# Kernel optimization log

Measured on AMD Instinct MI355X. Metric: run time of the kernel, lower is better.

## Reference

```python
import jax, jax.numpy as jnp
import numpy as np

B, S, H, DH = 2, 2048, 16, 64
DIM = H * DH          # 1024
WIN = 512             # relpos_win_size
LN_EPS = 1e-5


def setup_inputs() -> dict:
    key = jax.random.key(0)
    ks = jax.random.split(key, 8)
    return {
        "q": jax.random.normal(ks[0], (B, S, H, DH), dtype=jnp.float32),
        "k": jax.random.normal(ks[1], (B, S, H, DH), dtype=jnp.float32),
        "relpos_emb": jax.random.normal(ks[2], (WIN, DIM), dtype=jnp.float32),
        "ln_scale": jnp.ones((DIM,), dtype=jnp.float32),
        "ln_bias": jnp.zeros((DIM,), dtype=jnp.float32),
        "Wq": jax.random.normal(ks[3], (DIM, DIM), dtype=jnp.float32),
        "bq": jnp.zeros((DIM,), dtype=jnp.float32),
        "Wk": jax.random.normal(ks[4], (DIM, DIM), dtype=jnp.float32),
        "bk": jnp.zeros((DIM,), dtype=jnp.float32),
    }


def reference(q, k, relpos_emb, ln_scale, ln_bias, Wq, bq, Wk, bk):
    b, nq, h, dh = q.shape
    nk = k.shape[1]
    win = relpos_emb.shape[0]

    # LayerNorm over the embedding dim (use_pos_layer_norm=True); dropout is identity (eval).
    mu = jnp.mean(relpos_emb, axis=-1, keepdims=True)
    var = jnp.mean(jnp.square(relpos_emb - mu), axis=-1, keepdims=True)
    pe = (relpos_emb - mu) * jax.lax.rsqrt(var + LN_EPS) * ln_scale + ln_bias

    qpos = jnp.arange(nq)
    kpos = jnp.arange(nk)
    rel = jnp.clip(kpos[None, :] - qpos[:, None], -(win - 1), 0) + (win - 1)
    idx = jnp.broadcast_to(rel[None, None, :, :], (b, h, nq, nk))

    # Linear projections of the (small) relpos table, split into heads.
    relpos_k = (pe @ Wk.T + bk).reshape(win, h, dh)  # relpos_k_proj
    relpos_q = (pe @ Wq.T + bq).reshape(win, h, dh)  # relpos_q_proj

    # query-to-position: scores over window then gather along window axis (dim 3).
    query_pos_scores = jnp.einsum('bnhx,khx->bhnk', q, relpos_k)
    logits_query_pos = jnp.take_along_axis(query_pos_scores, idx, axis=3)  # [b,h,nq,nk]

    key_pos_scores = jnp.einsum('bnhx,khx->bhkn', k, relpos_q)
    logits_pos_key = jnp.take_along_axis(key_pos_scores, idx, axis=2)      # [b,h,nq,nk]

    # scale_factor = 1 + True + True = 3 (static constant, omitted from array outputs)
    return logits_pos_key, logits_query_pos, relpos_q, relpos_k
```

## Files before the change

kernel.cpp:

```cpp
#include <hip/hip_runtime.h>

#define BB 2
#define S 2048
#define H 16
#define DH 64
#define DIM 1024
#define WIN 512

#define OUT_PK 0
#define OUT_QP 134217728
#define OUT_RQ 268435456
#define OUT_RK 268959744

#define WS_C0Q   1024
#define WS_C511Q (1024 + 65536)
#define WS_C0K   (1024 + 2*65536)
#define WS_C511K (1024 + 3*65536)
#define WS_BF_BASE 263168

typedef short bf16x8 __attribute__((ext_vector_type(8)));
typedef float f32x4 __attribute__((ext_vector_type(4)));

__device__ inline short f2bf(float f) {
    union { float f; unsigned int u; } cv; cv.f = f;
    unsigned int u = cv.u + 0x7FFFu + ((cv.u >> 16) & 1u);
    return (short)(u >> 16);
}

__device__ inline float bf2f(short s) {
    union { unsigned int u; float f; } cv;
    cv.u = ((unsigned int)(unsigned short)s) << 16;
    return cv.f;
}

__global__ __launch_bounds__(256) void proj(const float* __restrict__ emb,
        const float* __restrict__ lnsc, const float* __restrict__ lnbi,
        const float* __restrict__ Wq, const float* __restrict__ bq,
        const float* __restrict__ Wk, const float* __restrict__ bk,
        float* __restrict__ out, short* __restrict__ rqbf, short* __restrict__ rkbf) {
    const float* W    = blockIdx.z ? Wk : Wq;
    const float* bias = blockIdx.z ? bk : bq;
    float* o = out + (blockIdx.z ? OUT_RK : OUT_RQ);
    short* bfo = blockIdx.z ? rkbf : rqbf;
    int r0 = blockIdx.x * 64;
    int d0 = blockIdx.y * 64;
    __shared__ short As[64 * 72];
    __shared__ short Bs[64 * 72];
    __shared__ float smu[64];
    __shared__ float srs[64];
    int t = threadIdx.x;

    {
        int rr = t >> 2, p = t & 3;
        const float4* rp = reinterpret_cast<const float4*>(emb + (r0 + rr) * DIM + p * 256);
        float s = 0.f, sq = 0.f;
#pragma unroll
        for (int i = 0; i < 64; ++i) {
            float4 v = rp[i];
            s  += v.x + v.y + v.z + v.w;
            sq += v.x * v.x + v.y * v.y + v.z * v.z + v.w * v.w;
        }
        s += __shfl_xor(s, 1); sq += __shfl_xor(sq, 1);
        s += __shfl_xor(s, 2); sq += __shfl_xor(sq, 2);
        if (p == 0) {
            float mu = s / DIM;
            float var = sq / DIM - mu * mu;
            smu[rr] = mu;
            srs[rr] = rsqrtf(var + 1e-5f);
        }
    }
    __syncthreads();

    int lane = t & 63, w = t >> 6, lr = lane & 15, lg = lane >> 4;
    int srow = t >> 2, seg = (t & 3) * 16;
    float mu = smu[srow], rs = srs[srow];

    f32x4 acc[4] = {};
    for (int c0 = 0; c0 < DIM; c0 += 64) {
        const float4* ep = reinterpret_cast<const float4*>(emb + (size_t)(r0 + srow) * DIM + c0 + seg);
        const float4* wp = reinterpret_cast<const float4*>(W + (size_t)(d0 + srow) * DIM + c0 + seg);
        short4* ad = reinterpret_cast<short4*>(&As[srow * 72 + seg]);
        short4* wd = reinterpret_cast<short4*>(&Bs[srow * 72 + seg]);
#pragma unroll
        for (int i = 0; i < 4; ++i) {
            float4 v = ep[i], wv = wp[i];
            int cb = c0 + seg + i * 4;
            float4 sc = *reinterpret_cast<const float4*>(lnsc + cb);
            float4 bi = *reinterpret_cast<const float4*>(lnbi + cb);
            short4 a4 = { f2bf((v.x - mu) * rs * sc.x + bi.x),
                          f2bf((v.y - mu) * rs * sc.y + bi.y),
                          f2bf((v.z - mu) * rs * sc.z + bi.z),
                          f2bf((v.w - mu) * rs * sc.w + bi.w) };
            short4 w4 = { f2bf(wv.x), f2bf(wv.y), f2bf(wv.z), f2bf(wv.w) };
            ad[i] = a4;
            wd[i] = w4;
        }
        __syncthreads();
#pragma unroll
        for (int kk = 0; kk < 2; ++kk) {
            bf16x8 a = *reinterpret_cast<const bf16x8*>(&As[(w * 16 + lr) * 72 + kk * 32 + lg * 8]);
#pragma unroll
            for (int cg = 0; cg < 4; ++cg) {
                bf16x8 b = *reinterpret_cast<const bf16x8*>(&Bs[(cg * 16 + lr) * 72 + kk * 32 + lg * 8]);
                acc[cg] = __builtin_amdgcn_mfma_f32_16x16x32_bf16(a, b, acc[cg], 0, 0, 0);
            }
        }
        __syncthreads();
    }
#pragma unroll
    for (int cg = 0; cg < 4; ++cg) {
        int col = d0 + cg * 16 + lr;
        float bv = bias[col];
        int hh = col >> 6, cc = col & 63;
#pragma unroll
        for (int reg = 0; reg < 4; ++reg) {
            int rr = r0 + w * 16 + lg * 4 + reg;
            float val = acc[cg][reg] + bv;
            o[(size_t)rr * DIM + col] = val;
            bfo[((size_t)(hh * 512) + rr) * 64 + cc] = f2bf(val);
        }
    }
}

__global__ __launch_bounds__(256) void qkprep(const float* __restrict__ q,
        const float* __restrict__ k, const float* __restrict__ out_ro,
        float* __restrict__ ws, short* __restrict__ qbf, short* __restrict__ kbf) {
    int z = blockIdx.z;
    int bh = blockIdx.y; int b = bh >> 4, h = bh & 15;
    int row = blockIdx.x * 64 + (threadIdx.x >> 2);
    int seg = (threadIdx.x & 3) * 16;
    const float* X = z ? k : q;
    const float* T = out_ro + (z ? OUT_RQ : OUT_RK);
    short* dst = z ? kbf : qbf;
    const float4* xp = reinterpret_cast<const float4*>(X + (size_t)((b * S + row) * H + h) * DH + seg);
    const float4* t0 = reinterpret_cast<const float4*>(T + h * DH + seg);
    const float4* t1 = reinterpret_cast<const float4*>(T + 511 * DIM + h * DH + seg);
    float d0 = 0.f, d1 = 0.f;
    short* dbase = dst + ((size_t)bh * 2048 + row) * 64 + seg;
#pragma unroll
    for (int i = 0; i < 4; ++i) {
        float4 x = xp[i], a = t0[i], c = t1[i];
        d0 += x.x * a.x + x.y * a.y + x.z * a.z + x.w * a.w;
        d1 += x.x * c.x + x.y * c.y + x.z * c.z + x.w * c.w;
        short4 o = { f2bf(x.x), f2bf(x.y), f2bf(x.z), f2bf(x.w) };
        *reinterpret_cast<short4*>(dbase + i * 4) = o;
    }
    d0 += __shfl_xor(d0, 1); d0 += __shfl_xor(d0, 2);
    d1 += __shfl_xor(d1, 1); d1 += __shfl_xor(d1, 2);
    if ((threadIdx.x & 3) == 0) {
        int o = bh * S + row;
        if (!z) { ws[WS_C0Q + o] = d0; ws[WS_C511Q + o] = d1; }
        else    { ws[WS_C0K + o] = d0; ws[WS_C511K + o] = d1; }
    }
}

__global__ __launch_bounds__(256) void outk(const short* __restrict__ qbf,
        const short* __restrict__ kbf, const short* __restrict__ rqbf,
        const short* __restrict__ rkbf, const float* __restrict__ ws,
        float* __restrict__ out) {
    __shared__ short Yt[64 * 132];

    int bid = blockIdx.x;
    int wg = (bid & 7) * 8192 + (bid >> 3);
    int PK = wg >> 15;
    int bh = (wg >> 10) & 31; int h = bh & 15;
    int nt = (wg >> 5) & 31, jt = wg & 31;
    int n0 = nt * 64, j0 = jt * 64;
    int jlo = nt > 8 ? nt - 8 : 0;
    int t = threadIdx.x;
    float* obase = out + (PK ? OUT_PK : OUT_QP) + (size_t)bh * S * S;

    if (jt < jlo || jt > nt) {
        int left = jt < jlo;
        const float* cv = ws + (PK ? (left ? WS_C0K : WS_C511K)
                                   : (left ? WS_C0Q : WS_C511Q)) + bh * S;
        int col4 = t & 15, r0w = t >> 4;
        if (PK) {
            f32x4 v = *reinterpret_cast<const f32x4*>(cv + j0 + col4 * 4);
#pragma unroll
            for (int i = 0; i < 4; ++i) {
                int n = n0 + r0w + i * 16;
                __builtin_nontemporal_store(v,
                    reinterpret_cast<f32x4*>(obase + (size_t)n * S + j0 + col4 * 4));
            }
        } else {
#pragma unroll
            for (int i = 0; i < 4; ++i) {
                int n = n0 + r0w + i * 16;
                float vs = cv[n];
                f32x4 v = { vs, vs, vs, vs };
                __builtin_nontemporal_store(v,
                    reinterpret_cast<f32x4*>(obase + (size_t)n * S + j0 + col4 * 4));
            }
        }
        return;
    }

    int rlo = 511 + j0 - (n0 + 63); rlo = rlo < 0 ? 0 : rlo;

    const short* xb = (PK ? kbf : qbf) + ((size_t)bh * 2048 + (PK ? j0 : n0)) * 64;
    const short* tbase = (PK ? rqbf : rkbf) + (size_t)h * 512 * 64;

    int lane = t & 63, w = t >> 6, lr = lane & 15, lg = lane >> 4;
    const short* arow = xb + (w * 16 + lr) * 64 + lg * 8;
    bf16x8 a0 = *reinterpret_cast<const bf16x8*>(arow);
    bf16x8 a1 = *reinterpret_cast<const bf16x8*>(arow + 32);

    bf16x8 b0s[8], b1s[8];
#pragma unroll
    for (int s = 0; s < 8; ++s) {
        int trow = rlo + s * 16 + lr;
        trow = trow > 511 ? 511 : trow;
        const short* brow = tbase + trow * 64 + lg * 8;
        b0s[s] = *reinterpret_cast<const bf16x8*>(brow);
        b1s[s] = *reinterpret_cast<const bf16x8*>(brow + 32);
    }
#pragma unroll
    for (int s = 0; s < 8; ++s) {
        f32x4 acc = {0.f, 0.f, 0.f, 0.f};
        acc = __builtin_amdgcn_mfma_f32_16x16x32_bf16(a0, b0s[s], acc, 0, 0, 0);
        acc = __builtin_amdgcn_mfma_f32_16x16x32_bf16(a1, b1s[s], acc, 0, 0, 0);
#pragma unroll
        for (int reg = 0; reg < 4; ++reg)
            Yt[(w * 16 + lg * 4 + reg) * 132 + s * 16 + lr] = f2bf(acc[reg]);
    }
    __syncthreads();

    int tx = t & 15, ty = t >> 4;
#pragma unroll
    for (int i = 0; i < 4; ++i) {
        int rowi = ty + i * 16;
        int n = n0 + rowi;
        float vv[4];
#pragma unroll
        for (int jj = 0; jj < 4; ++jj) {
            int j = j0 + tx * 4 + jj;
            int rel = 511 + j - n;
            rel = rel < 0 ? 0 : (rel > 511 ? 511 : rel);
            int g = rel - rlo;
            int m = PK ? (tx * 4 + jj) : rowi;
            vv[jj] = bf2f(Yt[m * 132 + g]);
        }
        f32x4 v = { vv[0], vv[1], vv[2], vv[3] };
        __builtin_nontemporal_store(v,
            reinterpret_cast<f32x4*>(obase + (size_t)n * S + j0 + tx * 4));
    }
}

extern "C" void kernel_launch(void* const* d_in, const int* in_sizes, int n_in,
                              void* d_out, int out_size, void* d_ws, size_t ws_size,
                              hipStream_t stream) {
    const float* q    = (const float*)d_in[0];
    const float* k    = (const float*)d_in[1];
    const float* emb  = (const float*)d_in[2];
    const float* lnsc = (const float*)d_in[3];
    const float* lnbi = (const float*)d_in[4];
    const float* Wq   = (const float*)d_in[5];
    const float* bq   = (const float*)d_in[6];
    const float* Wk   = (const float*)d_in[7];
    const float* bk   = (const float*)d_in[8];
    float* out = (float*)d_out;
    float* ws  = (float*)d_ws;

    short* qbf  = (short*)(ws + WS_BF_BASE);
    short* kbf  = qbf + (size_t)4194304;
    short* rqbf = kbf + (size_t)4194304;
    short* rkbf = rqbf + (size_t)524288;

    proj<<<dim3(8, 16, 2), dim3(256), 0, stream>>>(emb, lnsc, lnbi, Wq, bq, Wk, bk, out, rqbf, rkbf);
    qkprep<<<dim3(32, 32, 2), dim3(256), 0, stream>>>(q, k, out, ws, qbf, kbf);
    outk<<<dim3(65536), dim3(256), 0, stream>>>(qbf, kbf, rqbf, rkbf, ws, out);
}
```

Measured before the change: 234.6 us.

## Restructure work split: merge q/k bf16 conversion into projection, flat-fill row blocks

The q/k bf16 conversion now runs in the same launch as the relpos projection, and the edge-value dot products move to a separate small kernel that reads the bf16 copies. The output kernel now launches only band tiles (enumerated triangularly) plus flat work items that each fill the constant regions of 8 full rows, instead of one block per 64x64 tile. The LDS scratch tile is transposed so each lane writes a packed short4. This is meant to cut launch count and per-block overhead on the large constant-fill region. In exchange the edge values are now computed from bf16 inputs rather than fp32, which loses some precision.

Measured after the change: 310.6 us. +32.4%, slower.

```diff
diff --git a/kernel.cpp b/kernel.cpp
--- a/kernel.cpp
+++ b/kernel.cpp
@@ -33,22 +33,44 @@
     return cv.f;
 }
 
-__global__ __launch_bounds__(256) void proj(const float* __restrict__ emb,
+__global__ __launch_bounds__(256) void prep1(const float* __restrict__ emb,
         const float* __restrict__ lnsc, const float* __restrict__ lnbi,
         const float* __restrict__ Wq, const float* __restrict__ bq,
         const float* __restrict__ Wk, const float* __restrict__ bk,
-        float* __restrict__ out, short* __restrict__ rqbf, short* __restrict__ rkbf) {
-    const float* W    = blockIdx.z ? Wk : Wq;
-    const float* bias = blockIdx.z ? bk : bq;
-    float* o = out + (blockIdx.z ? OUT_RK : OUT_RQ);
-    short* bfo = blockIdx.z ? rkbf : rqbf;
-    int r0 = blockIdx.x * 64;
-    int d0 = blockIdx.y * 64;
+        const float* __restrict__ q, const float* __restrict__ k,
+        float* __restrict__ out, short* __restrict__ rqbf, short* __restrict__ rkbf,
+        short* __restrict__ qbf, short* __restrict__ kbf) {
     __shared__ short As[64 * 72];
     __shared__ short Bs[64 * 72];
     __shared__ float smu[64];
     __shared__ float srs[64];
+    int bid = blockIdx.x;
     int t = threadIdx.x;
+
+    if (bid >= 256) {
+        int cb = bid - 256;
+        int z = cb >> 10;
+        int blk = cb & 1023;
+        const float* src = z ? k : q;
+        short* dst = z ? kbf : qbf;
+        int e0 = (blk * 256 + t) * 16;
+        int c = e0 & 63, hh = (e0 >> 6) & 15, n = (e0 >> 10) & 2047, b = e0 >> 21;
+        short* dbase = dst + (((size_t)(b * 16 + hh) * 2048) + n) * 64 + c;
+#pragma unroll
+        for (int i = 0; i < 4; ++i) {
+            float4 v = *reinterpret_cast<const float4*>(src + e0 + i * 4);
+            short4 o = { f2bf(v.x), f2bf(v.y), f2bf(v.z), f2bf(v.w) };
+            *reinterpret_cast<short4*>(dbase + i * 4) = o;
+        }
+        return;
+    }
+
+    const float* W    = (bid >> 7) ? Wk : Wq;
+    const float* bias = (bid >> 7) ? bk : bq;
+    float* o = out + ((bid >> 7) ? OUT_RK : OUT_RQ);
+    short* bfo = (bid >> 7) ? rkbf : rqbf;
+    int r0 = (bid & 7) * 64;
+    int d0 = ((bid >> 3) & 15) * 64;
 
     {
         int rr = t >> 2, p = t & 3;
@@ -84,9 +106,9 @@
 #pragma unroll
         for (int i = 0; i < 4; ++i) {
             float4 v = ep[i], wv = wp[i];
-            int cb = c0 + seg + i * 4;
-            float4 sc = *reinterpret_cast<const float4*>(lnsc + cb);
-            float4 bi = *reinterpret_cast<const float4*>(lnbi + cb);
+            int cb2 = c0 + seg + i * 4;
+            float4 sc = *reinterpret_cast<const float4*>(lnsc + cb2);
+            float4 bi = *reinterpret_cast<const float4*>(lnbi + cb2);
             short4 a4 = { f2bf((v.x - mu) * rs * sc.x + bi.x),
                           f2bf((v.y - mu) * rs * sc.y + bi.y),
                           f2bf((v.z - mu) * rs * sc.z + bi.z),
@@ -122,33 +144,36 @@
     }
 }
 
-__global__ __launch_bounds__(256) void qkprep(const float* __restrict__ q,
-        const float* __restrict__ k, const float* __restrict__ out_ro,
-        float* __restrict__ ws, short* __restrict__ qbf, short* __restrict__ kbf) {
-    int z = blockIdx.z;
-    int bh = blockIdx.y; int b = bh >> 4, h = bh & 15;
-    int row = blockIdx.x * 64 + (threadIdx.x >> 2);
-    int seg = (threadIdx.x & 3) * 16;
-    const float* X = z ? k : q;
-    const float* T = out_ro + (z ? OUT_RQ : OUT_RK);
-    short* dst = z ? kbf : qbf;
-    const float4* xp = reinterpret_cast<const float4*>(X + (size_t)((b * S + row) * H + h) * DH + seg);
-    const float4* t0 = reinterpret_cast<const float4*>(T + h * DH + seg);
-    const float4* t1 = reinterpret_cast<const float4*>(T + 511 * DIM + h * DH + seg);
+__global__ __launch_bounds__(256) void cvec(const short* __restrict__ qbf,
+        const short* __restrict__ kbf, const short* __restrict__ rqbf,
+        const short* __restrict__ rkbf, float* __restrict__ ws) {
+    int cid = blockIdx.x;
+    int z = cid >> 10;
+    int rem = cid & 1023;
+    int bh = rem >> 5, rb = rem & 31;
+    int t = threadIdx.x;
+    int rr = t >> 2, p = t & 3;
+    int n = rb * 64 + rr;
+    int h = bh & 15;
+    const short* X = (z ? kbf : qbf) + ((size_t)bh * 2048 + n) * 64 + p * 16;
+    const short* T = (z ? rqbf : rkbf) + (size_t)h * 512 * 64 + p * 16;
+    bf16x8 x0 = *reinterpret_cast<const bf16x8*>(X);
+    bf16x8 x1 = *reinterpret_cast<const bf16x8*>(X + 8);
+    bf16x8 a0 = *reinterpret_cast<const bf16x8*>(T);
+    bf16x8 a1 = *reinterpret_cast<const bf16x8*>(T + 8);
+    bf16x8 c0 = *reinterpret_cast<const bf16x8*>(T + 511 * 64);
+    bf16x8 c1 = *reinterpret_cast<const bf16x8*>(T + 511 * 64 + 8);
     float d0 = 0.f, d1 = 0.f;
-    short* dbase = dst + ((size_t)bh * 2048 + row) * 64 + seg;
-#pragma unroll
-    for (int i = 0; i < 4; ++i) {
-        float4 x = xp[i], a = t0[i], c = t1[i];
-        d0 += x.x * a.x + x.y * a.y + x.z * a.z + x.w * a.w;
-        d1 += x.x * c.x + x.y * c.y + x.z * c.z + x.w * c.w;
-        short4 o = { f2bf(x.x), f2bf(x.y), f2bf(x.z), f2bf(x.w) };
-        *reinterpret_cast<short4*>(dbase + i * 4) = o;
+#pragma unroll
+    for (int e = 0; e < 8; ++e) {
+        float xa = bf2f(x0[e]), xb = bf2f(x1[e]);
+        d0 += xa * bf2f(a0[e]) + xb * bf2f(a1[e]);
+        d1 += xa * bf2f(c0[e]) + xb * bf2f(c1[e]);
     }
     d0 += __shfl_xor(d0, 1); d0 += __shfl_xor(d0, 2);
     d1 += __shfl_xor(d1, 1); d1 += __shfl_xor(d1, 2);
-    if ((threadIdx.x & 3) == 0) {
-        int o = bh * S + row;
+    if (p == 0) {
+        int o = bh * S + n;
         if (!z) { ws[WS_C0Q + o] = d0; ws[WS_C511Q + o] = d1; }
         else    { ws[WS_C0K + o] = d0; ws[WS_C511K + o] = d1; }
     }
@@ -158,45 +183,83 @@
         const short* __restrict__ kbf, const short* __restrict__ rqbf,
         const short* __restrict__ rkbf, const float* __restrict__ ws,
         float* __restrict__ out) {
-    __shared__ short Yt[64 * 132];
+    __shared__ short Yt[128 * 68];
 
     int bid = blockIdx.x;
-    int wg = (bid & 7) * 8192 + (bid >> 3);
-    int PK = wg >> 15;
-    int bh = (wg >> 10) & 31; int h = bh & 15;
-    int nt = (wg >> 5) & 31, jt = wg & 31;
+    int wid = (bid & 7) * 4064 + (bid >> 3);
+    int t = threadIdx.x;
+
+    int isflat, fid = 0, bnd = 0;
+    if (wid < 32256) { isflat = !(wid & 1); if (isflat) fid = wid >> 1; else bnd = wid >> 1; }
+    else             { isflat = 1; fid = 16128 + (wid - 32256); }
+
+    if (isflat) {
+        int PK = fid >> 13;
+        int rem = fid & 8191;
+        int bh = rem >> 8, rg = rem & 255;
+        int n0 = rg * 8, nt = n0 >> 6;
+        int jlo = nt > 8 ? nt - 8 : 0;
+        int jL4 = jlo << 4;
+        int jR = (nt + 1) << 6;
+        int nr4 = (2048 - jR) >> 2;
+        float* obase = out + (PK ? OUT_PK : OUT_QP) + (size_t)bh * S * S;
+        const float* c0 = ws + (PK ? WS_C0K : WS_C0Q) + bh * S;
+        const float* c1 = ws + (PK ? WS_C511K : WS_C511Q) + bh * S;
+        if (PK) {
+            for (int j4 = t; j4 < jL4; j4 += 256) {
+                f32x4 v = *reinterpret_cast<const f32x4*>(c0 + j4 * 4);
+#pragma unroll
+                for (int i = 0; i < 8; ++i)
+                    __builtin_nontemporal_store(v,
+                        reinterpret_cast<f32x4*>(obase + (size_t)(n0 + i) * S + j4 * 4));
+            }
+            for (int j4 = t; j4 < nr4; j4 += 256) {
+                f32x4 v = *reinterpret_cast<const f32x4*>(c1 + jR + j4 * 4);
+#pragma unroll
+                for (int i = 0; i < 8; ++i)
+                    __builtin_nontemporal_store(v,
+                        reinterpret_cast<f32x4*>(obase + (size_t)(n0 + i) * S + jR + j4 * 4));
+            }
+        } else {
+            float v0[8], v1[8];
+#pragma unroll
+            for (int i = 0; i < 8; ++i) { v0[i] = c0[n0 + i]; v1[i] = c1[n0 + i]; }
+            for (int j4 = t; j4 < jL4; j4 += 256) {
+#pragma unroll
+                for (int i = 0; i < 8; ++i) {
+                    f32x4 v = { v0[i], v0[i], v0[i], v0[i] };
+                    __builtin_nontemporal_store(v,
+                        reinterpret_cast<f32x4*>(obase + (size_t)(n0 + i) * S + j4 * 4));
+                }
+            }
+            for (int j4 = t; j4 < nr4; j4 += 256) {
+#pragma unroll
+                for (int i = 0; i < 8; ++i) {
+                    f32x4 v = { v1[i], v1[i], v1[i], v1[i] };
+                    __builtin_nontemporal_store(v,
+                        reinterpret_cast<f32x4*>(obase + (size_t)(n0 + i) * S + jR + j4 * 4));
+                }
+            }
+        }
+        return;
+    }
+
+    int sb = bnd / 252, r = bnd % 252;
+    int PK = sb >> 5, bh = sb & 31, h = bh & 15;
+    int nt, jt;
+    if (r < 45) {
+        nt = (int)((sqrtf(8.0f * r + 1.0f) - 1.0f) * 0.5f);
+        while ((nt + 1) * (nt + 2) / 2 <= r) ++nt;
+        while (nt * (nt + 1) / 2 > r) --nt;
+        jt = r - nt * (nt + 1) / 2;
+    } else {
+        int r2 = r - 45;
+        nt = 9 + r2 / 9;
+        jt = nt - 8 + r2 % 9;
+    }
     int n0 = nt * 64, j0 = jt * 64;
-    int jlo = nt > 8 ? nt - 8 : 0;
-    int t = threadIdx.x;
+    int rlo = 511 + j0 - (n0 + 63); rlo = rlo < 0 ? 0 : rlo;
     float* obase = out + (PK ? OUT_PK : OUT_QP) + (size_t)bh * S * S;
-
-    if (jt < jlo || jt > nt) {
-        int left = jt < jlo;
-        const float* cv = ws + (PK ? (left ? WS_C0K : WS_C511K)
-                                   : (left ? WS_C0Q : WS_C511Q)) + bh * S;
-        int col4 = t & 15, r0w = t >> 4;
-        if (PK) {
-            f32x4 v = *reinterpret_cast<const f32x4*>(cv + j0 + col4 * 4);
-#pragma unroll
-            for (int i = 0; i < 4; ++i) {
-                int n = n0 + r0w + i * 16;
-                __builtin_nontemporal_store(v,
-                    reinterpret_cast<f32x4*>(obase + (size_t)n * S + j0 + col4 * 4));
-            }
-        } else {
-#pragma unroll
-            for (int i = 0; i < 4; ++i) {
-                int n = n0 + r0w + i * 16;
-                float vs = cv[n];
-                f32x4 v = { vs, vs, vs, vs };
-                __builtin_nontemporal_store(v,
-                    reinterpret_cast<f32x4*>(obase + (size_t)n * S + j0 + col4 * 4));
-            }
-        }
-        return;
-    }
-
-    int rlo = 511 + j0 - (n0 + 63); rlo = rlo < 0 ? 0 : rlo;
 
     const short* xb = (PK ? kbf : qbf) + ((size_t)bh * 2048 + (PK ? j0 : n0)) * 64;
     const short* tbase = (PK ? rqbf : rkbf) + (size_t)h * 512 * 64;
@@ -220,9 +283,8 @@
         f32x4 acc = {0.f, 0.f, 0.f, 0.f};
         acc = __builtin_amdgcn_mfma_f32_16x16x32_bf16(a0, b0s[s], acc, 0, 0, 0);
         acc = __builtin_amdgcn_mfma_f32_16x16x32_bf16(a1, b1s[s], acc, 0, 0, 0);
-#pragma unroll
-        for (int reg = 0; reg < 4; ++reg)
-            Yt[(w * 16 + lg * 4 + reg) * 132 + s * 16 + lr] = f2bf(acc[reg]);
+        short4 pk4 = { f2bf(acc[0]), f2bf(acc[1]), f2bf(acc[2]), f2bf(acc[3]) };
+        *reinterpret_cast<short4*>(&Yt[(s * 16 + lr) * 68 + w * 16 + lg * 4]) = pk4;
     }
     __syncthreads();
 
@@ -239,7 +301,7 @@
             rel = rel < 0 ? 0 : (rel > 511 ? 511 : rel);
             int g = rel - rlo;
             int m = PK ? (tx * 4 + jj) : rowi;
-            vv[jj] = bf2f(Yt[m * 132 + g]);
+            vv[jj] = bf2f(Yt[g * 68 + m]);
         }
         f32x4 v = { vv[0], vv[1], vv[2], vv[3] };
         __builtin_nontemporal_store(v,
@@ -267,7 +329,8 @@
     short* rqbf = kbf + (size_t)4194304;
     short* rkbf = rqbf + (size_t)524288;
 
-    proj<<<dim3(8, 16, 2), dim3(256), 0, stream>>>(emb, lnsc, lnbi, Wq, bq, Wk, bk, out, rqbf, rkbf);
-    qkprep<<<dim3(32, 32, 2), dim3(256), 0, stream>>>(q, k, out, ws, qbf, kbf);
-    outk<<<dim3(65536), dim3(256), 0, stream>>>(qbf, kbf, rqbf, rkbf, ws, out);
-}
+    prep1<<<dim3(2304), dim3(256), 0, stream>>>(emb, lnsc, lnbi, Wq, bq, Wk, bk,
+                                                q, k, out, rqbf, rkbf, qbf, kbf);
+    cvec<<<dim3(2048), dim3(256), 0, stream>>>(qbf, kbf, rqbf, rkbf, ws);
+    outk<<<dim3(32512), dim3(256), 0, stream>>>(qbf, kbf, rqbf, rkbf, ws, out);
+}
```
